# Optimization experiments

Hardware: AMD Instinct MI355X
Metric: run time of the kernel (lower is better)

The kernel has to match this reference:

```python
import jax, jax.numpy as jnp
import numpy as np

B, T, E, V, L = 8, 128, 256, 8192, 5  # batch, block_size, embedding_size (== num heads, head_size=1), vocab, num blocks


def setup_inputs() -> dict:
    key = jax.random.key(0)
    ks = jax.random.split(key, 12)
    s = 0.02
    return {
        "idxs": jax.random.randint(ks[0], (B, T), 0, V),
        "targets": jax.random.randint(ks[1], (B, T), 0, V),
        "emb": jax.random.normal(ks[2], (V, E)) * s,
        "pos_emb": jax.random.normal(ks[3], (T, E)) * s,
        "Wq": jax.random.normal(ks[4], (L, E, E)) * s,  # per-layer: E heads, each Linear(E,1); columns are heads
        "Wk": jax.random.normal(ks[5], (L, E, E)) * s,
        "Wv": jax.random.normal(ks[6], (L, E, E)) * s,
        "Wfc": jax.random.normal(ks[7], (L, E, E)) * s,
        "bfc": jnp.zeros((L, E)),
        "Wlm": jax.random.normal(ks[8], (E, V)) * s,
        "blm": jnp.zeros((V,)),
    }


def _block(x, Wq, Wk, Wv, Wfc, bfc):
    # E heads of head_size=1: projecting with [E,E] gives [B,T,H] with H==E,
    # column h being head h's scalar q/k/v. Faithful to per-head Linear(E,1).
    q = x @ Wq
    k = x @ Wk
    v = x @ Wv
    scores = jnp.einsum('bih,bjh->bhij', q, k)  # no 1/sqrt(d) scaling (faithful)
    i = jnp.arange(x.shape[1])
    causal = i[:, None] >= i[None, :]  # masked_fill where tril==0, i.e. j>i -> -inf
    scores = jnp.where(causal[None, None], scores, -jnp.inf)
    attn = jax.nn.softmax(scores, axis=-2)  # NOTE: source softmaxes over dim=-2 (query axis) -- faithful quirk
    out = jnp.einsum('bhij,bjh->bih', attn, v)  # concat of heads == H axis order
    x = x + out
    return x + jax.nn.relu(x @ Wfc + bfc)


def reference(idxs, targets, emb, pos_emb, Wq, Wk, Wv, Wfc, bfc, Wlm, blm):
    x = emb[idxs] + pos_emb[: idxs.shape[1]]  # [B,T,E]
    for l in range(L):
        x = _block(x, Wq[l], Wk[l], Wv[l], Wfc[l], bfc[l])
    logits = (x @ Wlm + blm).reshape(-1, V)  # [B*T, V], as source views before CE
    logp = jax.nn.log_softmax(logits, axis=-1)
    loss = -jnp.take_along_axis(logp, targets.reshape(-1, 1), axis=-1).mean()
    return logits, loss
```

## Files before the change

kernel.cpp:

```cpp
#include <hip/hip_runtime.h>

#define BB 8
#define TT 128
#define EE 256
#define VV 8192
#define LL 5
#define NROWS (BB*TT)

typedef __attribute__((ext_vector_type(8))) short bf16x8;
typedef __attribute__((ext_vector_type(4))) float f32x4;

__device__ inline ushort f2bf(float f) {
    union { float f; unsigned u; } c; c.f = f;
    unsigned u = c.u;
    return (ushort)((u + 0x7FFF + ((u >> 16) & 1)) >> 16);
}

__global__ __launch_bounds__(256) void prep_kernel(
        const int* __restrict__ idxs, const float* __restrict__ emb, const float* __restrict__ pos,
        const float* __restrict__ Wq, const float* __restrict__ Wk,
        const float* __restrict__ Wv, const float* __restrict__ Wfc,
        const float* __restrict__ Wlm,
        float* __restrict__ x0, ushort* __restrict__ WTs, ushort* __restrict__ WlmT,
        float* __restrict__ loss_cell) {
    int id = blockIdx.x;
    if (id == 0) {
        if (threadIdx.x == 0) *loss_cell = 0.f;
        return;
    }
    if (id < 513) {
        __shared__ ushort ts[64][72];
        int idw = id - 1;
        int v0 = (idw & 127) * 64, k0 = (idw >> 7) * 64;
        int lane = threadIdx.x & 63, w = threadIdx.x >> 6;
        for (int kk = w; kk < 64; kk += 4)
            ts[lane][kk] = f2bf(Wlm[(size_t)(k0 + kk)*VV + v0 + lane]);
        __syncthreads();
        for (int vv = w; vv < 64; vv += 4)
            WlmT[(size_t)(v0 + vv)*EE + k0 + lane] = ts[vv][lane];
        return;
    }
    if (id < 833) {
        __shared__ ushort ts[64][72];
        int idm = id - 513;
        int mat = idm >> 4, tile = idm & 15;
        int l = mat >> 2, type = mat & 3;
        const float* src = (type == 0 ? Wq : type == 1 ? Wk : type == 2 ? Wv : Wfc) + l*EE*EE;
        ushort* dst = WTs + mat*EE*EE;
        int i0 = (tile >> 2) * 64, o0 = (tile & 3) * 64;
        int lane = threadIdx.x & 63, w = threadIdx.x >> 6;
        for (int ii = w; ii < 64; ii += 4)
            ts[lane][ii] = f2bf(src[(i0 + ii)*EE + o0 + lane]);
        __syncthreads();
        for (int oo = w; oo < 64; oo += 4)
            dst[(o0 + oo)*EE + i0 + lane] = ts[oo][lane];
        return;
    }
    int h = threadIdx.x;
    int row0 = (id - 833) * 4;
    for (int r = 0; r < 4; ++r) {
        int row = row0 + r;
        x0[row*EE + h] = emb[(size_t)idxs[row]*EE + h] + pos[(row & (TT-1))*EE + h];
    }
}

__global__ __launch_bounds__(512) void qkv_attn_kernel(
        float* __restrict__ x, const ushort* __restrict__ WTl) {
    __shared__ __align__(16) ushort Xs[128*256];
    __shared__ __align__(16) ushort Bs[32*256];
    __shared__ float QS[8*132], KS[8*132], VS[8*132], MS[8*132], RV[8*132];
    int tid = threadIdx.x, lane = tid & 63, w = tid >> 6;
    int b  = blockIdx.x >> 5;
    int h0 = (blockIdx.x & 31) * 8;

    for (int rr = w; rr < 128; rr += 8) {
        float4 v = *(const float4*)&x[(size_t)(b*TT + rr)*EE + lane*4];
        ushort4 hh; hh.x = f2bf(v.x); hh.y = f2bf(v.y); hh.z = f2bf(v.z); hh.w = f2bf(v.w);
        *(ushort4*)&Xs[rr*256 + ((lane*4) ^ ((rr & 7) << 3))] = hh;
    }
    {
        int c = tid >> 4;
        int kb = (tid & 15) * 16;
        uint4 v0 = make_uint4(0,0,0,0), v1 = v0;
        if (c < 24) {
            int mat = c >> 3;
            int col = h0 + (c & 7);
            const ushort* src = WTl + (size_t)mat*EE*EE + (size_t)col*EE + kb;
            v0 = *(const uint4*)&src[0];
            v1 = *(const uint4*)&src[8];
        }
        *(uint4*)&Bs[c*256 + (kb ^ ((c & 7) << 3))] = v0;
        *(uint4*)&Bs[c*256 + ((kb + 8) ^ ((c & 7) << 3))] = v1;
    }
    __syncthreads();

    {
        f32x4 acc[2] = {};
        int rband = w*16 + (lane & 15);
        int kq = (lane >> 4) * 8;
        for (int ks = 0; ks < 8; ++ks) {
            int kk = ks*32 + kq;
            bf16x8 a = *(const bf16x8*)&Xs[rband*256 + (kk ^ ((rband & 7) << 3))];
            #pragma unroll
            for (int ct = 0; ct < 2; ++ct) {
                int c = ct*16 + (lane & 15);
                bf16x8 bb = *(const bf16x8*)&Bs[c*256 + (kk ^ ((c & 7) << 3))];
                acc[ct] = __builtin_amdgcn_mfma_f32_16x16x32_bf16(a, bb, acc[ct], 0, 0, 0);
            }
        }
        int r_ = w*16 + ((lane >> 4) << 2);
        #pragma unroll
        for (int ct = 0; ct < 2; ++ct) {
            int col24 = ct*16 + (lane & 15);
            #pragma unroll
            for (int j = 0; j < 4; ++j) {
                float val = acc[ct][j];
                int row = r_ + j;
                if (col24 < 8)       QS[col24*132 + row] = val;
                else if (col24 < 16) KS[(col24-8)*132 + row] = val;
                else if (col24 < 24) VS[(col24-16)*132 + row] = val;
            }
        }
    }
    __syncthreads();

    int g = w, lg = lane;
    {
        int j0 = lg*2;
        float k0 = KS[g*132 + j0], k1 = KS[g*132 + j0 + 1];
        float q0j = QS[g*132 + j0], q1j = QS[g*132 + j0 + 1];
        float pmax = fmaxf(q0j, q1j), pmin = fminf(q0j, q1j);
        #pragma unroll
        for (int d = 1; d < 64; d <<= 1) {
            float om = __shfl_down(pmax, d);
            float on = __shfl_down(pmin, d);
            if (lg + d < 64) { pmax = fmaxf(pmax, om); pmin = fminf(pmin, on); }
        }
        float nx = __shfl_down(pmax, 1), nn = __shfl_down(pmin, 1);
        float sp1 = (lg == 63) ? q1j : fmaxf(q1j, nx);
        float sn1 = (lg == 63) ? q1j : fminf(q1j, nn);
        float m0 = (k0 >= 0.f) ? k0*pmax : k0*pmin;
        float m1 = (k1 >= 0.f) ? k1*sp1  : k1*sn1;
        float z0 = 0.f, z1 = 0.f;
        for (int i = j0; i < TT; ++i) {
            float qi = QS[g*132 + i];
            z0 += __expf(qi*k0 - m0);
            z1 += (i >= j0+1) ? __expf(qi*k1 - m1) : 0.f;
        }
        MS[g*132 + j0]     = m0;
        MS[g*132 + j0 + 1] = m1;
        RV[g*132 + j0]     = VS[g*132 + j0] / z0;
        RV[g*132 + j0 + 1] = VS[g*132 + j0 + 1] / z1;
    }
    __syncthreads();
    float a0 = 0.f, a1 = 0.f;
    {
        int i0 = lg*2;
        float q0 = QS[g*132 + i0], q1 = QS[g*132 + i0 + 1];
        for (int j = 0; j <= i0 + 1; ++j) {
            float kj = KS[g*132 + j], mj = MS[g*132 + j], rj = RV[g*132 + j];
            float e0 = __expf(q0*kj - mj) * rj;
            float e1 = __expf(q1*kj - mj) * rj;
            a0 += (j <= i0) ? e0 : 0.f;
            a1 += e1;
        }
    }
    __syncthreads();
    VS[g*132 + lg*2]     = a0;
    VS[g*132 + lg*2 + 1] = a1;
    __syncthreads();

    {
        int row = tid >> 2, cp = (tid & 3) * 2;
        size_t gx = (size_t)(b*TT + row)*EE + h0 + cp;
        float2 xv = *(float2*)&x[gx];
        xv.x += VS[cp*132 + row];
        xv.y += VS[(cp+1)*132 + row];
        *(float2*)&x[gx] = xv;
    }
}

__global__ __launch_bounds__(256) void fc_mfma(
        const float* __restrict__ xin, const ushort* __restrict__ WT,
        const float* __restrict__ bfc, float* __restrict__ xout) {
    __shared__ __align__(16) ushort As[64*256];
    __shared__ __align__(16) ushort Bs[64*256];
    int tid = threadIdx.x, lane = tid & 63, w = tid >> 6;
    int c0 = blockIdx.x * 64;
    int r0 = blockIdx.y * 64;

    for (int rr = w; rr < 64; rr += 4) {
        float4 v = *(const float4*)&xin[(size_t)(r0 + rr)*EE + lane*4];
        ushort4 hh; hh.x = f2bf(v.x); hh.y = f2bf(v.y); hh.z = f2bf(v.z); hh.w = f2bf(v.w);
        *(ushort4*)&As[rr*256 + ((lane*4) ^ ((rr & 7) << 3))] = hh;
    }
    for (int it = 0; it < 8; ++it) {
        int c = w*16 + (lane >> 5) + 2*it;
        int k0i = (lane & 31) * 8;
        uint4 v = *(const uint4*)&WT[(size_t)(c0 + c)*EE + k0i];
        *(uint4*)&Bs[c*256 + (k0i ^ ((c & 7) << 3))] = v;
    }
    __syncthreads();
    f32x4 acc[4] = {};
    int rband = w*16 + (lane & 15);
    int kq = (lane >> 4) * 8;
    for (int ks = 0; ks < 8; ++ks) {
        int kk = ks*32 + kq;
        bf16x8 a = *(const bf16x8*)&As[rband*256 + (kk ^ ((rband & 7) << 3))];
        #pragma unroll
        for (int n = 0; n < 4; ++n) {
            int c = n*16 + (lane & 15);
            bf16x8 b = *(const bf16x8*)&Bs[c*256 + (kk ^ ((c & 7) << 3))];
            acc[n] = __builtin_amdgcn_mfma_f32_16x16x32_bf16(a, b, acc[n], 0, 0, 0);
        }
    }
    int grow0 = r0 + w*16 + ((lane >> 4) << 2);
    #pragma unroll
    for (int n = 0; n < 4; ++n) {
        int col = c0 + n*16 + (lane & 15);
        float bias = bfc[col];
        #pragma unroll
        for (int j = 0; j < 4; ++j) {
            size_t idx = (size_t)(grow0 + j)*EE + col;
            xout[idx] = xin[idx] + fmaxf(acc[n][j] + bias, 0.f);
        }
    }
}

__global__ __launch_bounds__(512) void lm_mfma_kernel(
        const float* __restrict__ x, const ushort* __restrict__ WlmT,
        const float* __restrict__ blm, float* __restrict__ out,
        float* __restrict__ pm, float* __restrict__ pz) {
    __shared__ __align__(16) ushort LDSb[2*128*256];
    ushort* As = LDSb;
    ushort* Bs = LDSb + 128*256;
    int tid = threadIdx.x;
    int lane = tid & 63, w = tid >> 6;
    int c0 = blockIdx.x * 128;
    int r0 = blockIdx.y * 128;

    for (int rr = w; rr < 128; rr += 8) {
        float4 v = *(const float4*)&x[(size_t)(r0 + rr)*EE + lane*4];
        ushort4 hh; hh.x = f2bf(v.x); hh.y = f2bf(v.y); hh.z = f2bf(v.z); hh.w = f2bf(v.w);
        *(ushort4*)&As[rr*256 + ((lane*4) ^ ((rr & 7) << 3))] = hh;
    }
    for (int it = 0; it < 8; ++it) {
        int c = w*16 + (lane >> 5) + 2*it;
        int k0i = (lane & 31) * 8;
        uint4 v = *(const uint4*)&WlmT[(size_t)(c0 + c)*EE + k0i];
        *(uint4*)&Bs[c*256 + (k0i ^ ((c & 7) << 3))] = v;
    }
    __syncthreads();

    int wr = (w >> 2) * 64, wc = (w & 3) * 32;
    f32x4 acc[4][2] = {};
    int kq = (lane >> 4) * 8;
    for (int ks = 0; ks < 8; ++ks) {
        int kk = ks*32 + kq;
        bf16x8 a[4], bfr[2];
        #pragma unroll
        for (int m = 0; m < 4; ++m) {
            int rband = wr + m*16 + (lane & 15);
            a[m] = *(const bf16x8*)&As[rband*256 + (kk ^ ((rband & 7) << 3))];
        }
        #pragma unroll
        for (int n = 0; n < 2; ++n) {
            int c = wc + n*16 + (lane & 15);
            bfr[n] = *(const bf16x8*)&Bs[c*256 + (kk ^ ((c & 7) << 3))];
        }
        #pragma unroll
        for (int m = 0; m < 4; ++m)
            #pragma unroll
            for (int n = 0; n < 2; ++n)
                acc[m][n] = __builtin_amdgcn_mfma_f32_16x16x32_bf16(a[m], bfr[n], acc[m][n], 0, 0, 0);
    }
    __syncthreads();

    float* fst = (float*)LDSb;
    float bias[2];
    #pragma unroll
    for (int n = 0; n < 2; ++n) bias[n] = blm[c0 + wc + n*16 + (lane & 15)];
    #pragma unroll
    for (int m = 0; m < 4; ++m) {
        int rw = wr + m*16 + (lane >> 4)*4;
        #pragma unroll
        for (int j = 0; j < 4; ++j) {
            int row = rw + j;
            float vals[2];
            float vmax = -INFINITY;
            #pragma unroll
            for (int n = 0; n < 2; ++n) {
                vals[n] = acc[m][n][j] + bias[n];
                fst[row*132 + wc + n*16 + (lane & 15)] = vals[n];
                vmax = fmaxf(vmax, vals[n]);
            }
            #pragma unroll
            for (int msk = 1; msk <= 8; msk <<= 1) vmax = fmaxf(vmax, __shfl_xor(vmax, msk));
            float z = 0.f;
            #pragma unroll
            for (int n = 0; n < 2; ++n) z += __expf(vals[n] - vmax);
            #pragma unroll
            for (int msk = 1; msk <= 8; msk <<= 1) z += __shfl_xor(z, msk);
            if ((lane & 15) == 0) {
                pm[(size_t)(r0 + row)*256 + blockIdx.x*4 + (w & 3)] = vmax;
                pz[(size_t)(r0 + row)*256 + blockIdx.x*4 + (w & 3)] = z;
            }
        }
    }
    __syncthreads();
    #pragma unroll
    for (int it = 0; it < 8; ++it) {
        int k = tid + it*512;
        int row = k >> 5, c4 = (k & 31)*4;
        float4 v = *(float4*)&fst[row*132 + c4];
        *(float4*)&out[(size_t)(r0 + row)*VV + c0 + c4] = v;
    }
}

__global__ void loss_kernel(const float* __restrict__ pm, const float* __restrict__ pz,
                            const float* __restrict__ logits, const int* __restrict__ targets,
                            float* __restrict__ out_last) {
    int r = blockIdx.x;
    int t = threadIdx.x;
    __shared__ float sm[256], sz[256];
    float m = pm[(size_t)r*256 + t];
    float z = pz[(size_t)r*256 + t];
    sm[t] = m; __syncthreads();
    for (int s = 128; s > 0; s >>= 1) {
        if (t < s) sm[t] = fmaxf(sm[t], sm[t + s]);
        __syncthreads();
    }
    float M = sm[0];
    sz[t] = z * __expf(m - M); __syncthreads();
    for (int s = 128; s > 0; s >>= 1) {
        if (t < s) sz[t] += sz[t + s];
        __syncthreads();
    }
    if (t == 0) {
        float lse = M + logf(sz[0]);
        atomicAdd(out_last, (lse - logits[(size_t)r*VV + targets[r]]) * (1.0f / NROWS));
    }
}

extern "C" void kernel_launch(void* const* d_in, const int* in_sizes, int n_in,
                              void* d_out, int out_size, void* d_ws, size_t ws_size,
                              hipStream_t stream) {
    const int*   idxs    = (const int*)d_in[0];
    const int*   targets = (const int*)d_in[1];
    const float* emb     = (const float*)d_in[2];
    const float* pos     = (const float*)d_in[3];
    const float* Wq      = (const float*)d_in[4];
    const float* Wk      = (const float*)d_in[5];
    const float* Wv      = (const float*)d_in[6];
    const float* Wfc     = (const float*)d_in[7];
    const float* bfc     = (const float*)d_in[8];
    const float* Wlm     = (const float*)d_in[9];
    const float* blm     = (const float*)d_in[10];
    float* out = (float*)d_out;
    float* loss_cell = out + (size_t)NROWS * VV;

    float* ws = (float*)d_ws;
    float*  xa   = ws;
    float*  xb   = xa + NROWS*EE;
    float*  pm   = xb + NROWS*EE;
    float*  pz   = pm + NROWS*256;
    ushort* WTs  = (ushort*)(pz + NROWS*256);
    ushort* WlmT = WTs + 20*EE*EE;

    prep_kernel<<<1089, 256, 0, stream>>>(idxs, emb, pos, Wq, Wk, Wv, Wfc, Wlm,
                                          xa, WTs, WlmT, loss_cell);

    for (int l = 0; l < LL; ++l) {
        float* xi = (l & 1) ? xb : xa;
        float* xo = (l & 1) ? xa : xb;
        qkv_attn_kernel<<<256, 512, 0, stream>>>(xi, WTs + (size_t)l*4*EE*EE);
        fc_mfma<<<dim3(4, 16), 256, 0, stream>>>(xi, WTs + (size_t)(l*4 + 3)*EE*EE,
                                                 bfc + l*EE, xo);
    }

    lm_mfma_kernel<<<dim3(VV/128, NROWS/128), 512, 0, stream>>>(xb, WlmT, blm, out, pm, pz);
    loss_kernel<<<NROWS, 256, 0, stream>>>(pm, pz, out, targets, loss_cell);
}
```

Measured before the change: 208.1 us.

## Split K dimension into two halves to shrink LDS and raise occupancy

The QKV/attention kernel and the LM-head GEMM kernel now stage X and weight tiles in two K-halves of 128 instead of the full 256. This halves their LDS footprint (LM kernel reuses the buffer as the fp32 staging area) and adds launch_bounds min-blocks hints so more workgroups can reside per CU. The cost is an extra barrier and reload phase per kernel, with no overlap between loading and compute. A leftover empty block remains in the LM kernel.

```diff
diff --git a/kernel.cpp b/kernel.cpp
--- a/kernel.cpp
+++ b/kernel.cpp
@@ -64,50 +64,55 @@
     }
 }
 
-__global__ __launch_bounds__(512) void qkv_attn_kernel(
+__global__ __launch_bounds__(512, 4) void qkv_attn_kernel(
         float* __restrict__ x, const ushort* __restrict__ WTl) {
-    __shared__ __align__(16) ushort Xs[128*256];
-    __shared__ __align__(16) ushort Bs[32*256];
+    __shared__ __align__(16) ushort Xs[128*128];
+    __shared__ __align__(16) ushort Bs[32*128];
     __shared__ float QS[8*132], KS[8*132], VS[8*132], MS[8*132], RV[8*132];
     int tid = threadIdx.x, lane = tid & 63, w = tid >> 6;
     int b  = blockIdx.x >> 5;
     int h0 = (blockIdx.x & 31) * 8;
 
-    for (int rr = w; rr < 128; rr += 8) {
-        float4 v = *(const float4*)&x[(size_t)(b*TT + rr)*EE + lane*4];
-        ushort4 hh; hh.x = f2bf(v.x); hh.y = f2bf(v.y); hh.z = f2bf(v.z); hh.w = f2bf(v.w);
-        *(ushort4*)&Xs[rr*256 + ((lane*4) ^ ((rr & 7) << 3))] = hh;
-    }
-    {
-        int c = tid >> 4;
-        int kb = (tid & 15) * 16;
-        uint4 v0 = make_uint4(0,0,0,0), v1 = v0;
-        if (c < 24) {
-            int mat = c >> 3;
-            int col = h0 + (c & 7);
-            const ushort* src = WTl + (size_t)mat*EE*EE + (size_t)col*EE + kb;
-            v0 = *(const uint4*)&src[0];
-            v1 = *(const uint4*)&src[8];
-        }
-        *(uint4*)&Bs[c*256 + (kb ^ ((c & 7) << 3))] = v0;
-        *(uint4*)&Bs[c*256 + ((kb + 8) ^ ((c & 7) << 3))] = v1;
-    }
-    __syncthreads();
-
-    {
-        f32x4 acc[2] = {};
-        int rband = w*16 + (lane & 15);
-        int kq = (lane >> 4) * 8;
-        for (int ks = 0; ks < 8; ++ks) {
+    f32x4 acc[2] = {};
+    int rband = w*16 + (lane & 15);
+    int kq = (lane >> 4) * 8;
+
+    #pragma unroll
+    for (int half = 0; half < 2; ++half) {
+        if (half) __syncthreads();
+        {
+            int rsub = lane >> 5, cb = (lane & 31) * 4;
+            for (int rr2 = w*2; rr2 < 128; rr2 += 16) {
+                int rr = rr2 + rsub;
+                float4 v = *(const float4*)&x[(size_t)(b*TT + rr)*EE + half*128 + cb];
+                ushort4 hh; hh.x = f2bf(v.x); hh.y = f2bf(v.y); hh.z = f2bf(v.z); hh.w = f2bf(v.w);
+                *(ushort4*)&Xs[rr*128 + (cb ^ ((rr & 7) << 3))] = hh;
+            }
+        }
+        {
+            int c = tid >> 4;
+            int kb = (tid & 15) * 8;
+            uint4 v0 = make_uint4(0,0,0,0);
+            if (c < 24) {
+                int mat = c >> 3;
+                int col = h0 + (c & 7);
+                v0 = *(const uint4*)&WTl[(size_t)mat*EE*EE + (size_t)col*EE + half*128 + kb];
+            }
+            *(uint4*)&Bs[c*128 + (kb ^ ((c & 7) << 3))] = v0;
+        }
+        __syncthreads();
+        for (int ks = 0; ks < 4; ++ks) {
             int kk = ks*32 + kq;
-            bf16x8 a = *(const bf16x8*)&Xs[rband*256 + (kk ^ ((rband & 7) << 3))];
+            bf16x8 a = *(const bf16x8*)&Xs[rband*128 + (kk ^ ((rband & 7) << 3))];
             #pragma unroll
             for (int ct = 0; ct < 2; ++ct) {
                 int c = ct*16 + (lane & 15);
-                bf16x8 bb = *(const bf16x8*)&Bs[c*256 + (kk ^ ((c & 7) << 3))];
+                bf16x8 bb = *(const bf16x8*)&Bs[c*128 + (kk ^ ((c & 7) << 3))];
                 acc[ct] = __builtin_amdgcn_mfma_f32_16x16x32_bf16(a, bb, acc[ct], 0, 0, 0);
             }
         }
+    }
+    {
         int r_ = w*16 + ((lane >> 4) << 2);
         #pragma unroll
         for (int ct = 0; ct < 2; ++ct) {
@@ -227,56 +232,71 @@
     }
 }
 
-__global__ __launch_bounds__(512) void lm_mfma_kernel(
+__global__ __launch_bounds__(512, 4) void lm_mfma_kernel(
         const float* __restrict__ x, const ushort* __restrict__ WlmT,
         const float* __restrict__ blm, float* __restrict__ out,
         float* __restrict__ pm, float* __restrict__ pz) {
-    __shared__ __align__(16) ushort LDSb[2*128*256];
-    ushort* As = LDSb;
-    ushort* Bs = LDSb + 128*256;
+    __shared__ __align__(16) char LDSb[128*132*4];
+    ushort* As = (ushort*)LDSb;
+    ushort* Bs = (ushort*)LDSb + 128*128;
+    float*  fst = (float*)LDSb;
     int tid = threadIdx.x;
     int lane = tid & 63, w = tid >> 6;
     int c0 = blockIdx.x * 128;
     int r0 = blockIdx.y * 128;
 
-    for (int rr = w; rr < 128; rr += 8) {
-        float4 v = *(const float4*)&x[(size_t)(r0 + rr)*EE + lane*4];
-        ushort4 hh; hh.x = f2bf(v.x); hh.y = f2bf(v.y); hh.z = f2bf(v.z); hh.w = f2bf(v.w);
-        *(ushort4*)&As[rr*256 + ((lane*4) ^ ((rr & 7) << 3))] = hh;
-    }
-    for (int it = 0; it < 8; ++it) {
-        int c = w*16 + (lane >> 5) + 2*it;
-        int k0i = (lane & 31) * 8;
-        uint4 v = *(const uint4*)&WlmT[(size_t)(c0 + c)*EE + k0i];
-        *(uint4*)&Bs[c*256 + (k0i ^ ((c & 7) << 3))] = v;
-    }
-    __syncthreads();
-
     int wr = (w >> 2) * 64, wc = (w & 3) * 32;
     f32x4 acc[4][2] = {};
     int kq = (lane >> 4) * 8;
-    for (int ks = 0; ks < 8; ++ks) {
-        int kk = ks*32 + kq;
-        bf16x8 a[4], bfr[2];
-        #pragma unroll
-        for (int m = 0; m < 4; ++m) {
-            int rband = wr + m*16 + (lane & 15);
-            a[m] = *(const bf16x8*)&As[rband*256 + (kk ^ ((rband & 7) << 3))];
-        }
-        #pragma unroll
-        for (int n = 0; n < 2; ++n) {
-            int c = wc + n*16 + (lane & 15);
-            bfr[n] = *(const bf16x8*)&Bs[c*256 + (kk ^ ((c & 7) << 3))];
-        }
-        #pragma unroll
-        for (int m = 0; m < 4; ++m)
-            #pragma unroll
-            for (int n = 0; n < 2; ++n)
-                acc[m][n] = __builtin_amdgcn_mfma_f32_16x16x32_bf16(a[m], bfr[n], acc[m][n], 0, 0, 0);
-    }
-    __syncthreads();
-
-    float* fst = (float*)LDSb;
+
+    #pragma unroll
+    for (int half = 0; half < 2; ++half) {
+        if (half) __syncthreads();
+        {
+            int rsub = lane >> 5, cb = (lane & 31) * 4;
+            for (int rr2 = w*2; rr2 < 128; rr2 += 16) {
+                int rr = rr2 + rsub;
+                float4 v = *(const float4*)&x[(size_t)(r0 + rr)*EE + half*128 + cb];
+                ushort4 hh; hh.x = f2bf(v.x); hh.y = f2bf(v.y); hh.z = f2bf(v.z); hh.w = f2bf(v.w);
+                *(ushort4*)&As[rr*128 + (cb ^ ((rr & 7) << 3))] = hh;
+            }
+        }
+        {
+            int csub = lane >> 5, kb = (lane & 31) * 4;
+        }
+        {
+            int c = tid >> 4;
+            int kb = (tid & 15) * 8;
+            #pragma unroll
+            for (int cg = 0; cg < 4; ++cg) {
+                int cc = cg*32 + c;
+                uint4 v = *(const uint4*)&WlmT[(size_t)(c0 + cc)*EE + half*128 + kb];
+                *(uint4*)&Bs[cc*128 + (kb ^ ((cc & 7) << 3))] = v;
+            }
+        }
+        __syncthreads();
+        for (int ks = 0; ks < 4; ++ks) {
+            int kk = ks*32 + kq;
+            bf16x8 a[4], bfr[2];
+            #pragma unroll
+            for (int m = 0; m < 4; ++m) {
+                int rband = wr + m*16 + (lane & 15);
+                a[m] = *(const bf16x8*)&As[rband*128 + (kk ^ ((rband & 7) << 3))];
+            }
+            #pragma unroll
+            for (int n = 0; n < 2; ++n) {
+                int c = wc + n*16 + (lane & 15);
+                bfr[n] = *(const bf16x8*)&Bs[c*128 + (kk ^ ((c & 7) << 3))];
+            }
+            #pragma unroll
+            for (int m = 0; m < 4; ++m)
+                #pragma unroll
+                for (int n = 0; n < 2; ++n)
+                    acc[m][n] = __builtin_amdgcn_mfma_f32_16x16x32_bf16(a[m], bfr[n], acc[m][n], 0, 0, 0);
+        }
+    }
+    __syncthreads();
+
     float bias[2];
     #pragma unroll
     for (int n = 0; n < 2; ++n) bias[n] = blm[c0 + wc + n*16 + (lane & 15)];
```

Result: faster. 203.4 us (-2.2%).
